# Kernel optimization log

Measured on AMD Instinct MI355X. Metric: run time of the kernel, lower is better.

## Reference

```python
import jax, jax.numpy as jnp
import numpy as np

NEG_INF = -9e15  # same masking constant as the torch module


def setup_inputs() -> dict:
    key = jax.random.key(0)
    k1, k2, k3 = jax.random.split(key, 3)
    B, S, F = 8, 2048, 128
    H, D = 4, 32  # n_heads, head_dim = out_features // n_heads
    features = jax.random.normal(k1, (B, S, F), dtype=jnp.float32)
    adj_matrix = jax.random.randint(k2, (B, S, S), 0, 2, dtype=jnp.int32)
    # Xavier-uniform-ish init for W [H, F, D]
    limit = float(np.sqrt(6.0 / (F + D)))
    W = jax.random.uniform(k3, (H, F, D), dtype=jnp.float32, minval=-limit, maxval=limit)
    return {"features": features, "adj_matrix": adj_matrix, "W": W}


def reference(features, adj_matrix, W):
    # features: [B, S, F], adj_matrix: [B, S, S] (>0 == edge), W: [H, F, D]
    D = W.shape[-1]
    Wh = jnp.einsum("bsf,hfd->bhsd", features, W)                 # [B, H, S, D]
    scores = jnp.einsum("bhsd,bhtd->bhst", Wh, Wh) / jnp.sqrt(jnp.float32(D))
    scores = jnp.where(adj_matrix[:, None, :, :] > 0, scores, NEG_INF)
    attn = jax.nn.softmax(scores, axis=-1)                         # [B, H, S, S]
    # dropout is identity at inference (training=False)
    h = jnp.einsum("bhst,bhtd->bhsd", attn, Wh)                    # [B, H, S, D]
    B, H, S, _ = h.shape
    # concat heads along feature dim, matching torch.cat(heads, dim=2)
    return jnp.transpose(h, (0, 2, 1, 3)).reshape(B, S, H * D)
```

## Files before the change

kernel.cpp:

```cpp
#include <hip/hip_runtime.h>
#include <hip/hip_bf16.h>
#include <stdint.h>


namespace {
constexpr int S = 2048;
constexpr int F = 128;
constexpr int H = 4;
constexpr int D = 32;

typedef __attribute__((ext_vector_type(4))) float f32x4;
typedef __attribute__((ext_vector_type(8))) short s16x8;
typedef __attribute__((ext_vector_type(4))) short s16x4;

__device__ __forceinline__ short f2bf(float f) {
  __hip_bfloat16 h = __float2bfloat16(f);
  short s; __builtin_memcpy(&s, &h, sizeof(s)); return s;
}
__device__ __forceinline__ float bf2f(short s) {
  __hip_bfloat16 h; __builtin_memcpy(&h, &s, sizeof(s));
  return __bfloat162float(h);
}
__device__ __forceinline__ unsigned pkbf(float a, float b) {
  __hip_bfloat162 h = __float22bfloat162_rn(float2{a, b});
  unsigned u; __builtin_memcpy(&u, &h, 4); return u;
}
__device__ __forceinline__ s16x8 mkfrag(uint2 a, uint2 b) {
  union { unsigned u[4]; s16x8 s; } x;
  x.u[0] = a.x; x.u[1] = a.y; x.u[2] = b.x; x.u[3] = b.y;
  return x.s;
}

__global__ __launch_bounds__(256) void gat_proj(const float* __restrict__ feat,
                                                const float* __restrict__ W,
                                                short* __restrict__ Wh,
                                                short* __restrict__ WhT) {
  __shared__ __align__(16) short ftile[64][136];
  const int tid = threadIdx.x;
  const int w = tid >> 6;
  const int l = tid & 63;
  const int ln = l & 15, lg = l >> 4, g4 = (l >> 4) * 4;
  const int row0 = blockIdx.x * 64;
  const int b = row0 >> 11;
  const int sl0 = row0 & (S - 1);

#pragma unroll
  for (int i = 0; i < 4; ++i) {
    int c = i * 256 + tid;
    int r = c >> 4, c8 = (c & 15) * 8;
    const float* src = feat + (size_t)(row0 + r) * F + c8;
    float4 v0 = *(const float4*)src;
    float4 v1 = *(const float4*)(src + 4);
    s16x8 v;
    v[0]=f2bf(v0.x); v[1]=f2bf(v0.y); v[2]=f2bf(v0.z); v[3]=f2bf(v0.w);
    v[4]=f2bf(v1.x); v[5]=f2bf(v1.y); v[6]=f2bf(v1.z); v[7]=f2bf(v1.w);
    *(s16x8*)&ftile[r][c8] = v;
  }

  s16x8 bfr[4][2];
#pragma unroll
  for (int ks = 0; ks < 4; ++ks)
#pragma unroll
    for (int nt = 0; nt < 2; ++nt) {
      s16x8 v;
#pragma unroll
      for (int j = 0; j < 8; ++j)
        v[j] = f2bf(W[((size_t)w * F + ks*32 + lg*8 + j) * D + nt*16 + ln]);
      bfr[ks][nt] = v;
    }
  __syncthreads();

  const f32x4 z4 = {0.f, 0.f, 0.f, 0.f};
#pragma unroll
  for (int mt = 0; mt < 4; ++mt) {
    s16x8 a[4];
#pragma unroll
    for (int ks = 0; ks < 4; ++ks)
      a[ks] = *(const s16x8*)&ftile[mt*16 + ln][ks*32 + lg*8];
#pragma unroll
    for (int nt = 0; nt < 2; ++nt) {
      f32x4 c = z4;
#pragma unroll
      for (int ks = 0; ks < 4; ++ks)
        c = __builtin_amdgcn_mfma_f32_16x16x32_bf16(a[ks], bfr[ks][nt], c, 0, 0, 0);
      s16x4 tv;
#pragma unroll
      for (int r = 0; r < 4; ++r) {
        tv[r] = f2bf(c[r]);
        int srow = row0 + mt*16 + g4 + r;
        int s = srow & (S - 1);
        Wh[(((size_t)b * H + w) * S + s) * D + nt*16 + ln] = tv[r];
      }
      *(s16x4*)&WhT[(((size_t)b * H + w) * D + nt*16 + ln) * S + sl0 + mt*16 + g4] = tv;
    }
  }
}

__global__ __launch_bounds__(256, 4) void gat_attn(const int* __restrict__ adj,
                                                   const short* __restrict__ Wh,
                                                   const short* __restrict__ WhT,
                                                   float* __restrict__ out,
                                                   float* __restrict__ PO,
                                                   float* __restrict__ PS,
                                                   int tiles) {
  __shared__ __align__(16) unsigned short maskm[2][32][76];

  const int tid = threadIdx.x;
  const int w = tid >> 6;
  const int l = tid & 63;
  const int ln = l & 15, lg = l >> 4, g4 = (l >> 4) * 4;

  const int N = gridDim.x;
  const int rbid = ((int)blockIdx.x & 7) * (N >> 3) + ((int)blockIdx.x >> 3);
  const int c = rbid >> 9;
  const int g = rbid & 511;
  const int b = g >> 6;
  const int s0 = (g & 63) * 32;
  const int it0 = c * tiles;

  const short* WhBH = Wh + ((size_t)b * H + w) * S * D;
  const short* WhTBH = WhT + ((size_t)b * H + w) * D * S;

  const int arow = tid >> 3;
  const int gc = tid & 7;
  const int* adjTh = adj + (size_t)b * S * S + (size_t)(s0 + arow) * S
                     + (size_t)it0 * 64 + gc * 8;

  int toff[4];
#pragma unroll
  for (int mt = 0; mt < 4; ++mt)
    toff[mt] = 32*(mt >> 1) + 8*(ln >> 2) + 4*(mt & 1) + (ln & 3);

  const float cs = 0.25503486f;
  s16x8 qf[2];
#pragma unroll
  for (int qt = 0; qt < 2; ++qt) {
    s16x8 v = *(const s16x8*)&WhBH[(size_t)(s0 + qt*16 + ln) * D + lg*8];
    s16x8 o;
#pragma unroll
    for (int j = 0; j < 8; ++j) o[j] = f2bf(bf2f(v[j]) * cs);
    qf[qt] = o;
  }

  s16x8 onesf;
#pragma unroll
  for (int j = 0; j < 8; ++j) onesf[j] = (short)0x3F80;

  const f32x4 z4 = {0.f, 0.f, 0.f, 0.f};
  f32x4 accO[2][2];
  f32x4 accP[2];
#pragma unroll
  for (int i = 0; i < 2; ++i) {
    accP[i] = z4;
#pragma unroll
    for (int j = 0; j < 2; ++j) accO[i][j] = z4;
  }

  {
    int4 a0 = *(const int4*)adjTh;
    int4 a1 = *(const int4*)(adjTh + 4);
    uint2 u0, u1;
    u0.x = (a0.x ? 0xFFFFu : 0u) | (a0.y ? 0xFFFF0000u : 0u);
    u0.y = (a0.z ? 0xFFFFu : 0u) | (a0.w ? 0xFFFF0000u : 0u);
    u1.x = (a1.x ? 0xFFFFu : 0u) | (a1.y ? 0xFFFF0000u : 0u);
    u1.y = (a1.z ? 0xFFFFu : 0u) | (a1.w ? 0xFFFF0000u : 0u);
    *(uint2*)&maskm[0][arow][gc * 8] = u0;
    *(uint2*)&maskm[0][arow][gc * 8 + 4] = u1;
  }
  s16x8 kf[4];
  s16x8 av[2][2];
  {
    const size_t t0 = (size_t)it0 * 64;
#pragma unroll
    for (int mt = 0; mt < 4; ++mt)
      kf[mt] = *(const s16x8*)&WhBH[(t0 + toff[mt]) * D + lg*8];
#pragma unroll
    for (int dt = 0; dt < 2; ++dt)
#pragma unroll
      for (int kt = 0; kt < 2; ++kt)
        av[dt][kt] = *(const s16x8*)&WhTBH[(size_t)(dt*16 + ln) * S + t0 + kt*32 + lg*8];
  }
  __syncthreads();

#pragma unroll 1
  for (int i = 0; i < tiles; ++i) {
    const int cur = i & 1;
    const bool pf = (i + 1 < tiles);
    const int iLd = pf ? i + 1 : i;
    const size_t tnl = (size_t)(it0 + iLd) * 64;

    int4 a0n = *(const int4*)(adjTh + (size_t)iLd * 64);
    int4 a1n = *(const int4*)(adjTh + (size_t)iLd * 64 + 4);

    uint2 pks[2][4];
#pragma unroll
    for (int mt = 0; mt < 4; ++mt) {
      f32x4 sA = __builtin_amdgcn_mfma_f32_16x16x32_bf16(kf[mt], qf[0], z4, 0, 0, 0);
      f32x4 sB = __builtin_amdgcn_mfma_f32_16x16x32_bf16(kf[mt], qf[1], z4, 0, 0, 0);
      kf[mt] = *(const s16x8*)&WhBH[(tnl + toff[mt]) * D + lg*8];

      const int tb = 32*(mt >> 1) + 8*lg + 4*(mt & 1);
      uint2 mmA = *(const uint2*)&maskm[cur][ln][tb];
      uint2 mmB = *(const uint2*)&maskm[cur][16 + ln][tb];
      uint2 pa, pb;
      pa.x = pkbf(__builtin_amdgcn_exp2f(sA[0]), __builtin_amdgcn_exp2f(sA[1])) & mmA.x;
      pa.y = pkbf(__builtin_amdgcn_exp2f(sA[2]), __builtin_amdgcn_exp2f(sA[3])) & mmA.y;
      pb.x = pkbf(__builtin_amdgcn_exp2f(sB[0]), __builtin_amdgcn_exp2f(sB[1])) & mmB.x;
      pb.y = pkbf(__builtin_amdgcn_exp2f(sB[2]), __builtin_amdgcn_exp2f(sB[3])) & mmB.y;
      pks[0][mt] = pa;
      pks[1][mt] = pb;
    }

    s16x8 ap[2][2];
#pragma unroll
    for (int qt = 0; qt < 2; ++qt)
#pragma unroll
      for (int kt = 0; kt < 2; ++kt)
        ap[qt][kt] = mkfrag(pks[qt][2*kt], pks[qt][2*kt + 1]);

#pragma unroll
    for (int dt = 0; dt < 2; ++dt)
#pragma unroll
      for (int qt = 0; qt < 2; ++qt)
#pragma unroll
        for (int kt = 0; kt < 2; ++kt)
          accO[dt][qt] = __builtin_amdgcn_mfma_f32_16x16x32_bf16(
              av[dt][kt], ap[qt][kt], accO[dt][qt], 0, 0, 0);

#pragma unroll
    for (int dt = 0; dt < 2; ++dt)
#pragma unroll
      for (int kt = 0; kt < 2; ++kt)
        av[dt][kt] = *(const s16x8*)&WhTBH[(size_t)(dt*16 + ln) * S + tnl + kt*32 + lg*8];

#pragma unroll
    for (int qt = 0; qt < 2; ++qt)
#pragma unroll
      for (int kt = 0; kt < 2; ++kt)
        accP[qt] = __builtin_amdgcn_mfma_f32_16x16x32_bf16(
            onesf, ap[qt][kt], accP[qt], 0, 0, 0);

    if (pf) {
      uint2 u0, u1;
      u0.x = (a0n.x ? 0xFFFFu : 0u) | (a0n.y ? 0xFFFF0000u : 0u);
      u0.y = (a0n.z ? 0xFFFFu : 0u) | (a0n.w ? 0xFFFF0000u : 0u);
      u1.x = (a1n.x ? 0xFFFFu : 0u) | (a1n.y ? 0xFFFF0000u : 0u);
      u1.y = (a1n.z ? 0xFFFFu : 0u) | (a1n.w ? 0xFFFF0000u : 0u);
      *(uint2*)&maskm[cur ^ 1][arow][gc * 8] = u0;
      *(uint2*)&maskm[cur ^ 1][arow][gc * 8 + 4] = u1;
    }
    __syncthreads();
  }

  if (PO == nullptr) {
#pragma unroll
    for (int qt = 0; qt < 2; ++qt) {
      float inv = 1.0f / accP[qt][0];
#pragma unroll
      for (int dt = 0; dt < 2; ++dt) {
        f32x4 o;
#pragma unroll
        for (int r = 0; r < 4; ++r) o[r] = accO[dt][qt][r] * inv;
        *(f32x4*)&out[((size_t)b * S + s0 + qt*16 + ln) * (H * D) + w*32 + dt*16 + g4] = o;
      }
    }
  } else {
    const size_t pbase = (size_t)rbid * H + w;
    float* po = PO + pbase * 1024;
#pragma unroll
    for (int qt = 0; qt < 2; ++qt) {
#pragma unroll
      for (int dt = 0; dt < 2; ++dt)
        *(f32x4*)&po[(qt*16 + ln)*32 + dt*16 + g4] = accO[dt][qt];
      if (lg == 0) PS[pbase * 32 + qt*16 + ln] = accP[qt][0];
    }
  }
}

__global__ __launch_bounds__(256) void gat_reduce(const float* __restrict__ PO,
                                                  const float* __restrict__ PS,
                                                  float* __restrict__ out,
                                                  int nchunks) {
  const int f4 = blockIdx.x * 256 + threadIdx.x;
  const int d4 = f4 & 31;
  const int h = d4 >> 3;
  const int dq = d4 & 7;
  const int s_flat = f4 >> 5;
  const int b = s_flat >> 11, s = s_flat & 2047;
  const int g = b * 64 + (s >> 5), q = s & 31;

  f32x4 acc = {0.f, 0.f, 0.f, 0.f};
  float ps = 0.f;
  for (int c = 0; c < nchunks; ++c) {
    size_t pbase = ((size_t)(c * 512 + g)) * H + h;
    acc += *(const f32x4*)&PO[pbase * 1024 + q*32 + dq*4];
    ps += PS[pbase * 32 + q];
  }
  float inv = 1.0f / ps;
  f32x4 o = acc * inv;
  *(f32x4*)&out[(size_t)f4 * 4] = o;
}

}

extern "C" void kernel_launch(void* const* d_in, const int* in_sizes, int n_in,
                              void* d_out, int out_size, void* d_ws, size_t ws_size,
                              hipStream_t stream) {
  const float* feat = (const float*)d_in[0];
  const int* adj    = (const int*)d_in[1];
  const float* W    = (const float*)d_in[2];
  float* out        = (float*)d_out;

  short* Wh  = (short*)d_ws;
  short* WhT = Wh + (size_t)8 * H * S * D;
  const size_t whbytes = (size_t)2 * 8 * H * S * D * sizeof(short);
  const size_t chunkPO = (size_t)512 * H * 1024 * sizeof(float);
  const size_t chunkPS = (size_t)512 * H * 32 * sizeof(float);

  int nchunks = 1;
  if (ws_size >= whbytes + 2 * (chunkPO + chunkPS)) nchunks = 2;

  float* PO = nullptr;
  float* PS = nullptr;
  if (nchunks > 1) {
    PO = (float*)((char*)d_ws + whbytes);
    PS = (float*)((char*)d_ws + whbytes + (size_t)nchunks * chunkPO);
  }

  gat_proj<<<(8 * S) / 64, 256, 0, stream>>>(feat, W, Wh, WhT);
  gat_attn<<<512 * nchunks, 256, 0, stream>>>(adj, Wh, WhT, out, PO, PS, 32 / nchunks);
  if (nchunks > 1) gat_reduce<<<2048, 256, 0, stream>>>(PO, PS, out, nchunks);
}
```

Before: 73.32 us.

## Restructure attention into single-wave blocks looping over all heads per mask load

The attention kernel now uses one 64-thread wavefront per block that handles 16 query rows for all four heads. Each adjacency mask is loaded into registers once and reused across heads, which removes the shared-memory mask staging and the per-tile __syncthreads. Softmax row sums are accumulated in scalar registers from the packed bf16 probabilities rather than through an extra ones-matrix MFMA. The key split grows to four chunks when workspace allows, which means larger partial buffers and more reduce traffic in exchange for more parallel blocks.

```diff
diff --git a/kernel.cpp b/kernel.cpp
--- a/kernel.cpp
+++ b/kernel.cpp
@@ -29,6 +29,12 @@
   union { unsigned u[4]; s16x8 s; } x;
   x.u[0] = a.x; x.u[1] = a.y; x.u[2] = b.x; x.u[3] = b.y;
   return x.s;
+}
+__device__ __forceinline__ unsigned mk2(int x, int y) {
+  return (x ? 0xFFFFu : 0u) | (y ? 0xFFFF0000u : 0u);
+}
+__device__ __forceinline__ float upk(unsigned u) {
+  return __uint_as_float(u << 16) + __uint_as_float(u & 0xFFFF0000u);
 }
 
 __global__ __launch_bounds__(256) void gat_proj(const float* __restrict__ feat,
@@ -96,76 +102,66 @@
   }
 }
 
-__global__ __launch_bounds__(256, 4) void gat_attn(const int* __restrict__ adj,
-                                                   const short* __restrict__ Wh,
-                                                   const short* __restrict__ WhT,
-                                                   float* __restrict__ out,
-                                                   float* __restrict__ PO,
-                                                   float* __restrict__ PS,
-                                                   int tiles) {
-  __shared__ __align__(16) unsigned short maskm[2][32][76];
-
-  const int tid = threadIdx.x;
-  const int w = tid >> 6;
-  const int l = tid & 63;
-  const int ln = l & 15, lg = l >> 4, g4 = (l >> 4) * 4;
+__global__ __launch_bounds__(64) void gat_attn(const int* __restrict__ adj,
+                                               const short* __restrict__ Wh,
+                                               const short* __restrict__ WhT,
+                                               float* __restrict__ out,
+                                               float* __restrict__ PO,
+                                               float* __restrict__ PS,
+                                               int tiles) {
+  const int l = threadIdx.x;
+  const int ln = l & 15, lg = l >> 4;
 
   const int N = gridDim.x;
   const int rbid = ((int)blockIdx.x & 7) * (N >> 3) + ((int)blockIdx.x >> 3);
-  const int c = rbid >> 9;
-  const int g = rbid & 511;
-  const int b = g >> 6;
-  const int s0 = (g & 63) * 32;
+  const int c = rbid >> 10;
+  const int g = rbid & 1023;
+  const int b = g >> 7;
+  const int s0 = (g & 127) * 16;
   const int it0 = c * tiles;
 
-  const short* WhBH = Wh + ((size_t)b * H + w) * S * D;
-  const short* WhTBH = WhT + ((size_t)b * H + w) * D * S;
-
-  const int arow = tid >> 3;
-  const int gc = tid & 7;
-  const int* adjTh = adj + (size_t)b * S * S + (size_t)(s0 + arow) * S
-                     + (size_t)it0 * 64 + gc * 8;
+  const int4* adjL = (const int4*)(adj + (size_t)b * S * S + (size_t)(s0 + ln) * S);
+  const int aoff = 2 * lg;
 
   int toff[4];
 #pragma unroll
   for (int mt = 0; mt < 4; ++mt)
     toff[mt] = 32*(mt >> 1) + 8*(ln >> 2) + 4*(mt & 1) + (ln & 3);
 
+  const short* WhH[H];
+  const short* WhTH[H];
+#pragma unroll
+  for (int h = 0; h < H; ++h) {
+    WhH[h]  = Wh  + ((size_t)b * H + h) * S * D;
+    WhTH[h] = WhT + ((size_t)b * H + h) * D * S;
+  }
+
   const float cs = 0.25503486f;
-  s16x8 qf[2];
-#pragma unroll
-  for (int qt = 0; qt < 2; ++qt) {
-    s16x8 v = *(const s16x8*)&WhBH[(size_t)(s0 + qt*16 + ln) * D + lg*8];
+  s16x8 qf[H];
+#pragma unroll
+  for (int h = 0; h < H; ++h) {
+    s16x8 v = *(const s16x8*)&WhH[h][(size_t)(s0 + ln) * D + lg*8];
     s16x8 o;
 #pragma unroll
     for (int j = 0; j < 8; ++j) o[j] = f2bf(bf2f(v[j]) * cs);
-    qf[qt] = o;
-  }
-
-  s16x8 onesf;
-#pragma unroll
-  for (int j = 0; j < 8; ++j) onesf[j] = (short)0x3F80;
+    qf[h] = o;
+  }
 
   const f32x4 z4 = {0.f, 0.f, 0.f, 0.f};
-  f32x4 accO[2][2];
-  f32x4 accP[2];
-#pragma unroll
-  for (int i = 0; i < 2; ++i) {
-    accP[i] = z4;
-#pragma unroll
-    for (int j = 0; j < 2; ++j) accO[i][j] = z4;
-  }
-
+  f32x4 accO[H][2];
+  float psum[H] = {0.f, 0.f, 0.f, 0.f};
+#pragma unroll
+  for (int h = 0; h < H; ++h) { accO[h][0] = z4; accO[h][1] = z4; }
+
+  unsigned m[8];
   {
-    int4 a0 = *(const int4*)adjTh;
-    int4 a1 = *(const int4*)(adjTh + 4);
-    uint2 u0, u1;
-    u0.x = (a0.x ? 0xFFFFu : 0u) | (a0.y ? 0xFFFF0000u : 0u);
-    u0.y = (a0.z ? 0xFFFFu : 0u) | (a0.w ? 0xFFFF0000u : 0u);
-    u1.x = (a1.x ? 0xFFFFu : 0u) | (a1.y ? 0xFFFF0000u : 0u);
-    u1.y = (a1.z ? 0xFFFFu : 0u) | (a1.w ? 0xFFFF0000u : 0u);
-    *(uint2*)&maskm[0][arow][gc * 8] = u0;
-    *(uint2*)&maskm[0][arow][gc * 8 + 4] = u1;
+    const int base = it0 * 16 + aoff;
+    int4 a0 = adjL[base], a1 = adjL[base + 1];
+    int4 a2 = adjL[base + 8], a3 = adjL[base + 9];
+    m[0] = mk2(a0.x, a0.y); m[1] = mk2(a0.z, a0.w);
+    m[2] = mk2(a1.x, a1.y); m[3] = mk2(a1.z, a1.w);
+    m[4] = mk2(a2.x, a2.y); m[5] = mk2(a2.z, a2.w);
+    m[6] = mk2(a3.x, a3.y); m[7] = mk2(a3.z, a3.w);
   }
   s16x8 kf[4];
   s16x8 av[2][2];
@@ -173,106 +169,105 @@
     const size_t t0 = (size_t)it0 * 64;
 #pragma unroll
     for (int mt = 0; mt < 4; ++mt)
-      kf[mt] = *(const s16x8*)&WhBH[(t0 + toff[mt]) * D + lg*8];
+      kf[mt] = *(const s16x8*)&WhH[0][(t0 + toff[mt]) * D + lg*8];
 #pragma unroll
     for (int dt = 0; dt < 2; ++dt)
 #pragma unroll
       for (int kt = 0; kt < 2; ++kt)
-        av[dt][kt] = *(const s16x8*)&WhTBH[(size_t)(dt*16 + ln) * S + t0 + kt*32 + lg*8];
-  }
-  __syncthreads();
+        av[dt][kt] = *(const s16x8*)&WhTH[0][(size_t)(dt*16 + ln) * S + t0 + kt*32 + lg*8];
+  }
 
 #pragma unroll 1
   for (int i = 0; i < tiles; ++i) {
-    const int cur = i & 1;
-    const bool pf = (i + 1 < tiles);
-    const int iLd = pf ? i + 1 : i;
-    const size_t tnl = (size_t)(it0 + iLd) * 64;
-
-    int4 a0n = *(const int4*)(adjTh + (size_t)iLd * 64);
-    int4 a1n = *(const int4*)(adjTh + (size_t)iLd * 64 + 4);
-
-    uint2 pks[2][4];
-#pragma unroll
-    for (int mt = 0; mt < 4; ++mt) {
-      f32x4 sA = __builtin_amdgcn_mfma_f32_16x16x32_bf16(kf[mt], qf[0], z4, 0, 0, 0);
-      f32x4 sB = __builtin_amdgcn_mfma_f32_16x16x32_bf16(kf[mt], qf[1], z4, 0, 0, 0);
-      kf[mt] = *(const s16x8*)&WhBH[(tnl + toff[mt]) * D + lg*8];
-
-      const int tb = 32*(mt >> 1) + 8*lg + 4*(mt & 1);
-      uint2 mmA = *(const uint2*)&maskm[cur][ln][tb];
-      uint2 mmB = *(const uint2*)&maskm[cur][16 + ln][tb];
-      uint2 pa, pb;
-      pa.x = pkbf(__builtin_amdgcn_exp2f(sA[0]), __builtin_amdgcn_exp2f(sA[1])) & mmA.x;
-      pa.y = pkbf(__builtin_amdgcn_exp2f(sA[2]), __builtin_amdgcn_exp2f(sA[3])) & mmA.y;
-      pb.x = pkbf(__builtin_amdgcn_exp2f(sB[0]), __builtin_amdgcn_exp2f(sB[1])) & mmB.x;
-      pb.y = pkbf(__builtin_amdgcn_exp2f(sB[2]), __builtin_amdgcn_exp2f(sB[3])) & mmB.y;
-      pks[0][mt] = pa;
-      pks[1][mt] = pb;
-    }
-
-    s16x8 ap[2][2];
-#pragma unroll
-    for (int qt = 0; qt < 2; ++qt)
+    const int iLd = (i + 1 < tiles) ? i + 1 : i;
+    const size_t tc = (size_t)(it0 + i) * 64;
+    const size_t tn = (size_t)(it0 + iLd) * 64;
+
+    const int anb = (it0 + iLd) * 16 + aoff;
+    int4 a0n = adjL[anb],     a1n = adjL[anb + 1];
+    int4 a2n = adjL[anb + 8], a3n = adjL[anb + 9];
+
+#pragma unroll
+    for (int h = 0; h < H; ++h) {
+      f32x4 sv[4];
+#pragma unroll
+      for (int mt = 0; mt < 4; ++mt)
+        sv[mt] = __builtin_amdgcn_mfma_f32_16x16x32_bf16(kf[mt], qf[h], z4, 0, 0, 0);
+
+      {
+        const short* kb = (h < 3) ? WhH[h + 1] : WhH[0];
+        const size_t tk = (h < 3) ? tc : tn;
+#pragma unroll
+        for (int mt = 0; mt < 4; ++mt)
+          kf[mt] = *(const s16x8*)&kb[(tk + toff[mt]) * D + lg*8];
+      }
+
+      uint2 pks[4];
+#pragma unroll
+      for (int mt = 0; mt < 4; ++mt) {
+        uint2 pk;
+        pk.x = pkbf(__builtin_amdgcn_exp2f(sv[mt][0]),
+                    __builtin_amdgcn_exp2f(sv[mt][1])) & m[2*mt];
+        pk.y = pkbf(__builtin_amdgcn_exp2f(sv[mt][2]),
+                    __builtin_amdgcn_exp2f(sv[mt][3])) & m[2*mt + 1];
+        psum[h] += upk(pk.x) + upk(pk.y);
+        pks[mt] = pk;
+      }
+      s16x8 ap[2];
 #pragma unroll
       for (int kt = 0; kt < 2; ++kt)
-        ap[qt][kt] = mkfrag(pks[qt][2*kt], pks[qt][2*kt + 1]);
-
-#pragma unroll
-    for (int dt = 0; dt < 2; ++dt)
-#pragma unroll
-      for (int qt = 0; qt < 2; ++qt)
+        ap[kt] = mkfrag(pks[2*kt], pks[2*kt + 1]);
+
+#pragma unroll
+      for (int dt = 0; dt < 2; ++dt)
 #pragma unroll
         for (int kt = 0; kt < 2; ++kt)
-          accO[dt][qt] = __builtin_amdgcn_mfma_f32_16x16x32_bf16(
-              av[dt][kt], ap[qt][kt], accO[dt][qt], 0, 0, 0);
-
-#pragma unroll
-    for (int dt = 0; dt < 2; ++dt)
-#pragma unroll
-      for (int kt = 0; kt < 2; ++kt)
-        av[dt][kt] = *(const s16x8*)&WhTBH[(size_t)(dt*16 + ln) * S + tnl + kt*32 + lg*8];
-
-#pragma unroll
-    for (int qt = 0; qt < 2; ++qt)
-#pragma unroll
-      for (int kt = 0; kt < 2; ++kt)
-        accP[qt] = __builtin_amdgcn_mfma_f32_16x16x32_bf16(
-            onesf, ap[qt][kt], accP[qt], 0, 0, 0);
-
-    if (pf) {
-      uint2 u0, u1;
-      u0.x = (a0n.x ? 0xFFFFu : 0u) | (a0n.y ? 0xFFFF0000u : 0u);
-      u0.y = (a0n.z ? 0xFFFFu : 0u) | (a0n.w ? 0xFFFF0000u : 0u);
-      u1.x = (a1n.x ? 0xFFFFu : 0u) | (a1n.y ? 0xFFFF0000u : 0u);
-      u1.y = (a1n.z ? 0xFFFFu : 0u) | (a1n.w ? 0xFFFF0000u : 0u);
-      *(uint2*)&maskm[cur ^ 1][arow][gc * 8] = u0;
-      *(uint2*)&maskm[cur ^ 1][arow][gc * 8 + 4] = u1;
-    }
-    __syncthreads();
+          accO[h][dt] = __builtin_amdgcn_mfma_f32_16x16x32_bf16(
+              av[dt][kt], ap[kt], accO[h][dt], 0, 0, 0);
+
+      {
+        const short* vb = (h < 3) ? WhTH[h + 1] : WhTH[0];
+        const size_t tv = (h < 3) ? tc : tn;
+#pragma unroll
+        for (int dt = 0; dt < 2; ++dt)
+#pragma unroll
+          for (int kt = 0; kt < 2; ++kt)
+            av[dt][kt] = *(const s16x8*)&vb[(size_t)(dt*16 + ln) * S + tv + kt*32 + lg*8];
+      }
+    }
+
+    m[0] = mk2(a0n.x, a0n.y); m[1] = mk2(a0n.z, a0n.w);
+    m[2] = mk2(a1n.x, a1n.y); m[3] = mk2(a1n.z, a1n.w);
+    m[4] = mk2(a2n.x, a2n.y); m[5] = mk2(a2n.z, a2n.w);
+    m[6] = mk2(a3n.x, a3n.y); m[7] = mk2(a3n.z, a3n.w);
+  }
+
+#pragma unroll
+  for (int h = 0; h < H; ++h) {
+    psum[h] += __shfl_xor(psum[h], 16, 64);
+    psum[h] += __shfl_xor(psum[h], 32, 64);
   }
 
   if (PO == nullptr) {
 #pragma unroll
-    for (int qt = 0; qt < 2; ++qt) {
-      float inv = 1.0f / accP[qt][0];
+    for (int h = 0; h < H; ++h) {
+      float inv = 1.0f / psum[h];
 #pragma unroll
       for (int dt = 0; dt < 2; ++dt) {
         f32x4 o;
 #pragma unroll
-        for (int r = 0; r < 4; ++r) o[r] = accO[dt][qt][r] * inv;
-        *(f32x4*)&out[((size_t)b * S + s0 + qt*16 + ln) * (H * D) + w*32 + dt*16 + g4] = o;
+        for (int r = 0; r < 4; ++r) o[r] = accO[h][dt][r] * inv;
+        *(f32x4*)&out[((size_t)b * S + s0 + ln) * (H * D) + h*32 + dt*16 + 4*lg] = o;
       }
     }
   } else {
-    const size_t pbase = (size_t)rbid * H + w;
-    float* po = PO + pbase * 1024;
-#pragma unroll
-    for (int qt = 0; qt < 2; ++qt) {
+    float* po = PO + (size_t)rbid * 2048;
+#pragma unroll
+    for (int h = 0; h < H; ++h) {
 #pragma unroll
       for (int dt = 0; dt < 2; ++dt)
-        *(f32x4*)&po[(qt*16 + ln)*32 + dt*16 + g4] = accO[dt][qt];
-      if (lg == 0) PS[pbase * 32 + qt*16 + ln] = accP[qt][0];
+        *(f32x4*)&po[ln*128 + h*32 + dt*16 + 4*lg] = accO[h][dt];
+      if (lg == 0) PS[(size_t)rbid * 64 + h*16 + ln] = psum[h];
     }
   }
 }
@@ -284,17 +279,16 @@
   const int f4 = blockIdx.x * 256 + threadIdx.x;
   const int d4 = f4 & 31;
   const int h = d4 >> 3;
-  const int dq = d4 & 7;
   const int s_flat = f4 >> 5;
   const int b = s_flat >> 11, s = s_flat & 2047;
-  const int g = b * 64 + (s >> 5), q = s & 31;
+  const int s16 = s >> 4, q = s & 15;
 
   f32x4 acc = {0.f, 0.f, 0.f, 0.f};
   float ps = 0.f;
   for (int c = 0; c < nchunks; ++c) {
-    size_t pbase = ((size_t)(c * 512 + g)) * H + h;
-    acc += *(const f32x4*)&PO[pbase * 1024 + q*32 + dq*4];
-    ps += PS[pbase * 32 + q];
+    size_t rbid = (size_t)c * 1024 + b * 128 + s16;
+    acc += *(const f32x4*)&PO[rbid * 2048 + q*128 + d4*4];
+    ps += PS[rbid * 64 + h*16 + q];
   }
   float inv = 1.0f / ps;
   f32x4 o = acc * inv;
@@ -314,11 +308,12 @@
   short* Wh  = (short*)d_ws;
   short* WhT = Wh + (size_t)8 * H * S * D;
   const size_t whbytes = (size_t)2 * 8 * H * S * D * sizeof(short);
-  const size_t chunkPO = (size_t)512 * H * 1024 * sizeof(float);
-  const size_t chunkPS = (size_t)512 * H * 32 * sizeof(float);
+  const size_t chunkPO = (size_t)1024 * 2048 * sizeof(float);
+  const size_t chunkPS = (size_t)1024 * 64 * sizeof(float);
 
   int nchunks = 1;
-  if (ws_size >= whbytes + 2 * (chunkPO + chunkPS)) nchunks = 2;
+  if (ws_size >= whbytes + 4 * (chunkPO + chunkPS)) nchunks = 4;
+  else if (ws_size >= whbytes + 2 * (chunkPO + chunkPS)) nchunks = 2;
 
   float* PO = nullptr;
   float* PS = nullptr;
@@ -328,6 +323,6 @@
   }
 
   gat_proj<<<(8 * S) / 64, 256, 0, stream>>>(feat, W, Wh, WhT);
-  gat_attn<<<512 * nchunks, 256, 0, stream>>>(adj, Wh, WhT, out, PO, PS, 32 / nchunks);
+  gat_attn<<<1024 * nchunks, 64, 0, stream>>>(adj, Wh, WhT, out, PO, PS, 32 / nchunks);
   if (nchunks > 1) gat_reduce<<<2048, 256, 0, stream>>>(PO, PS, out, nchunks);
 }
```

New measurement: 128.1 us. 1.75x slower.
